# Kernel tuning notes

Measured on AMD Instinct MI355X. Metric: run time of the kernel, lower is better.

## Reference

```python
import jax, jax.numpy as jnp
import numpy as np

L, H, E, V, T_BLK = 8, 8, 768, 32000, 1024
B, T = 4, 1024
HS = E // H  # head size 96
STD = 0.02


def setup_inputs() -> dict:
    key = jax.random.key(0)
    ks = jax.random.split(key, 12)
    p = {}
    p["idx"] = jax.random.randint(ks[0], (B, T), 0, V)
    p["targets"] = jax.random.randint(ks[1], (B, T), 0, V)
    p["tok_emb"] = jax.random.normal(ks[2], (V, E), jnp.float32) * STD  # tied with lm_head
    p["pos_emb"] = jax.random.normal(ks[3], (T_BLK, E), jnp.float32) * STD
    p["Wq"] = jax.random.normal(ks[4], (L, E, E), jnp.float32) * STD
    p["Wk"] = jax.random.normal(ks[5], (L, E, E), jnp.float32) * STD
    p["Wv"] = jax.random.normal(ks[6], (L, E, E), jnp.float32) * STD
    p["Wo"] = jax.random.normal(ks[7], (L, E, E), jnp.float32) * STD
    p["bo"] = jnp.zeros((L, E), jnp.float32)
    p["ln1_g"] = jnp.ones((L, E), jnp.float32)
    p["ln1_b"] = jnp.zeros((L, E), jnp.float32)
    p["ln2_g"] = jnp.ones((L, E), jnp.float32)
    p["ln2_b"] = jnp.zeros((L, E), jnp.float32)
    p["W1"] = jax.random.normal(ks[8], (L, E, 4 * E), jnp.float32) * STD
    p["b1"] = jnp.zeros((L, 4 * E), jnp.float32)
    p["W2"] = jax.random.normal(ks[9], (L, 4 * E, E), jnp.float32) * STD
    p["b2"] = jnp.zeros((L, E), jnp.float32)
    p["lnf_g"] = jnp.ones((E,), jnp.float32)
    p["lnf_b"] = jnp.zeros((E,), jnp.float32)
    return p


def _ln(x, g, b):
    m = x.mean(-1, keepdims=True)
    v = ((x - m) ** 2).mean(-1, keepdims=True)
    return (x - m) * jax.lax.rsqrt(v + 1e-5) * g + b


def _attn(x, Wq, Wk, Wv, Wo, bo, mask):
    Bx, Tx, _ = x.shape
    q = (x @ Wq).reshape(Bx, Tx, H, HS)
    k = (x @ Wk).reshape(Bx, Tx, H, HS)
    v = (x @ Wv).reshape(Bx, Tx, H, HS)
    # per-head causal attention, scale by head_size**-0.5 as in source
    wei = jnp.einsum("bthd,bshd->bhts", q, k) * (HS ** -0.5)
    wei = jnp.where(mask, wei, -jnp.inf)
    wei = jax.nn.softmax(wei, axis=-1)
    out = jnp.einsum("bhts,bshd->bthd", wei, v).reshape(Bx, Tx, E)
    return out @ Wo + bo


def reference(idx, targets, tok_emb, pos_emb, Wq, Wk, Wv, Wo, bo,
              ln1_g, ln1_b, ln2_g, ln2_b, W1, b1, W2, b2, lnf_g, lnf_b):
    Tx = idx.shape[1]
    x = tok_emb[idx] + pos_emb[:Tx]  # [B,T,E]
    mask = jnp.tril(jnp.ones((Tx, Tx), bool))
    for l in range(L):
        x = x + _attn(_ln(x, ln1_g[l], ln1_b[l]), Wq[l], Wk[l], Wv[l], Wo[l], bo[l], mask)
        h = _ln(x, ln2_g[l], ln2_b[l])
        x = x + jax.nn.gelu(h @ W1[l] + b1[l], approximate=False) @ W2[l] + b2[l]
    x = _ln(x, lnf_g, lnf_b)
    logits = x @ tok_emb.T  # tied lm_head, [B,T,V]
    logp = jax.nn.log_softmax(logits, axis=-1)
    loss = -jnp.take_along_axis(logp, targets[..., None], axis=-1).mean()
    return logits, loss
```

## Files before the change

kernel.cpp:

```cpp
#include <hip/hip_runtime.h>
#include <cstdint>
#include <cstddef>


typedef __bf16 bf16_t;
typedef __bf16 bf16x8 __attribute__((ext_vector_type(8)));
typedef __bf16 bf16x4 __attribute__((ext_vector_type(4)));
typedef float  f32x4  __attribute__((ext_vector_type(4)));

#define LNUM 8
#define EMB 768
#define FFDIM 3072
#define HEADS 8
#define HSZ 96
#define VOC 32000
#define SEQ 1024
#define MTOK 4096
#define NT500 500

__device__ __forceinline__ void lds16(const void* g, void* l) {
    __builtin_amdgcn_global_load_lds(
        (__attribute__((address_space(1))) void*)(g),
        (__attribute__((address_space(3))) void*)(l), 16, 0, 0);
}

__global__ __launch_bounds__(256) void cast_bf16_kernel(
    const float* __restrict__ s, bf16_t* __restrict__ d, int n4)
{
    int i = blockIdx.x * 256 + threadIdx.x;
    if (i < n4) {
        float4 v = ((const float4*)s)[i];
        bf16x4 o;
        o[0] = (bf16_t)v.x; o[1] = (bf16_t)v.y;
        o[2] = (bf16_t)v.z; o[3] = (bf16_t)v.w;
        ((bf16x4*)d)[i] = o;
    }
}

__global__ __launch_bounds__(256) void transpose_cast_kernel(
    const float* __restrict__ src, bf16_t* __restrict__ dst,
    int K, int N, long long sstride, long long dstride)
{
    __shared__ float t[32][33];
    src += (long long)blockIdx.z * sstride;
    dst += (long long)blockIdx.z * dstride;
    int n0 = blockIdx.x * 32, k0 = blockIdx.y * 32;
    int tx = threadIdx.x, ty = threadIdx.y;
    for (int i = ty; i < 32; i += 8)
        t[i][tx] = src[(size_t)(k0 + i) * N + n0 + tx];
    __syncthreads();
    for (int i = ty; i < 32; i += 8)
        dst[(size_t)(n0 + i) * K + k0 + tx] = (bf16_t)t[tx][i];
}

__global__ __launch_bounds__(256) void embed_kernel(
    const int* __restrict__ idx, const float* __restrict__ tok,
    const float* __restrict__ pos, float* __restrict__ x)
{
    int row = blockIdx.x, tid = threadIdx.x;
    int id = idx[row];
    int t = row & (SEQ - 1);
    const float* te = tok + (size_t)id * EMB;
    const float* pe = pos + (size_t)t * EMB;
    float* xr = x + (size_t)row * EMB;
    xr[tid]       = te[tid]       + pe[tid];
    xr[tid + 256] = te[tid + 256] + pe[tid + 256];
    xr[tid + 512] = te[tid + 512] + pe[tid + 512];
}

__global__ __launch_bounds__(256) void ln_kernel(
    const float* __restrict__ x, const float* __restrict__ g,
    const float* __restrict__ bb, bf16_t* __restrict__ out)
{
    int row = blockIdx.x, tid = threadIdx.x;
    const float* xr = x + (size_t)row * EMB;
    float v0 = xr[tid], v1 = xr[tid + 256], v2 = xr[tid + 512];
    float s = v0 + v1 + v2;
    float s2 = v0 * v0 + v1 * v1 + v2 * v2;
#pragma unroll
    for (int off = 32; off >= 1; off >>= 1) {
        s  += __shfl_xor(s, off);
        s2 += __shfl_xor(s2, off);
    }
    __shared__ float red[8];
    int w = tid >> 6;
    if ((tid & 63) == 0) { red[w] = s; red[4 + w] = s2; }
    __syncthreads();
    s  = red[0] + red[1] + red[2] + red[3];
    s2 = red[4] + red[5] + red[6] + red[7];
    float mean = s * (1.0f / EMB);
    float var  = s2 * (1.0f / EMB) - mean * mean;
    float rs = rsqrtf(var + 1e-5f);
    bf16_t* orow = out + (size_t)row * EMB;
    orow[tid]       = (bf16_t)((v0 - mean) * rs * g[tid]       + bb[tid]);
    orow[tid + 256] = (bf16_t)((v1 - mean) * rs * g[tid + 256] + bb[tid + 256]);
    orow[tid + 512] = (bf16_t)((v2 - mean) * rs * g[tid + 512] + bb[tid + 512]);
}

__global__ __launch_bounds__(256) void gemm_nt_kernel(
    const bf16_t* __restrict__ A, const bf16_t* __restrict__ B,
    int N, int K, long long strideBz, long long strideOz,
    const float* __restrict__ bias, const float* __restrict__ resid,
    float* __restrict__ outF, bf16_t* __restrict__ outH, int gelu_flag,
    float* __restrict__ pmaxp, float* __restrict__ psump, int nt500)
{
    __shared__ __align__(16) bf16_t As[128 * 32];
    __shared__ __align__(16) bf16_t Bs[128 * 32];
    int tid = threadIdx.x;
    int m0 = blockIdx.y * 128;
    int n0 = blockIdx.x * 128;
    int z = blockIdx.z;
    B += (long long)z * strideBz;

    int wv = tid >> 6, lane = tid & 63;
    int quad = lane >> 4, l16 = lane & 15;
    int wm = wv >> 1, wn = wv & 1;

    const bf16_t* gA0 = A + (size_t)(m0 + (tid >> 2)) * K + (tid & 3) * 8;
    const bf16_t* gA1 = gA0 + (size_t)64 * K;
    const bf16_t* gB0 = B + (size_t)(n0 + (tid >> 2)) * K + (tid & 3) * 8;
    const bf16_t* gB1 = gB0 + (size_t)64 * K;
    bf16_t* lA0 = As + (wv << 9);
    bf16_t* lA1 = lA0 + 2048;
    bf16_t* lB0 = Bs + (wv << 9);
    bf16_t* lB1 = lB0 + 2048;

    f32x4 acc[4][4];
#pragma unroll
    for (int i = 0; i < 4; i++)
#pragma unroll
        for (int j = 0; j < 4; j++) {
            f32x4 zz = {0.f, 0.f, 0.f, 0.f};
            acc[i][j] = zz;
        }

    const bf16_t* fa = As + (wm * 64 + l16) * 32 + quad * 8;
    const bf16_t* fb = Bs + (wn * 64 + l16) * 32 + quad * 8;

    for (int kt = 0; kt < K; kt += 32) {
        lds16(gA0 + kt, lA0);
        lds16(gA1 + kt, lA1);
        lds16(gB0 + kt, lB0);
        lds16(gB1 + kt, lB1);
        __syncthreads();
        bf16x8 af[4], bfr[4];
#pragma unroll
        for (int i = 0; i < 4; i++) {
            af[i]  = *(const bf16x8*)(fa + i * 512);
            bfr[i] = *(const bf16x8*)(fb + i * 512);
        }
#pragma unroll
        for (int i = 0; i < 4; i++)
#pragma unroll
            for (int j = 0; j < 4; j++)
                acc[i][j] = __builtin_amdgcn_mfma_f32_16x16x32_bf16(
                    af[i], bfr[j], acc[i][j], 0, 0, 0);
        __syncthreads();
    }

    int mbase = m0 + wm * 64 + quad * 4;
    int nbase = n0 + wn * 64 + l16;

    if (outH) {
        bf16_t* oh = outH + (long long)z * strideOz;
#pragma unroll
        for (int i = 0; i < 4; i++)
#pragma unroll
            for (int j = 0; j < 4; j++) {
                int col = nbase + j * 16;
                float bv = bias ? bias[col] : 0.f;
#pragma unroll
                for (int r = 0; r < 4; r++) {
                    int row = mbase + i * 16 + r;
                    float v = acc[i][j][r] + bv;
                    if (gelu_flag)
                        v = 0.5f * v * (1.f + erff(v * 0.70710678118654752f));
                    oh[(size_t)row * N + col] = (bf16_t)v;
                }
            }
    } else {
#pragma unroll
        for (int i = 0; i < 4; i++)
#pragma unroll
            for (int j = 0; j < 4; j++) {
                int col = nbase + j * 16;
                float bv = bias ? bias[col] : 0.f;
#pragma unroll
                for (int r = 0; r < 4; r++) {
                    int row = mbase + i * 16 + r;
                    float v = acc[i][j][r] + bv;
                    if (resid) v += resid[(size_t)row * N + col];
                    outF[(size_t)row * N + col] = v;
                }
            }
        if (pmaxp) {
            int nt = blockIdx.x * 2 + wn;
#pragma unroll
            for (int i = 0; i < 4; i++)
#pragma unroll
                for (int r = 0; r < 4; r++) {
                    int row = mbase + i * 16 + r;
                    float mx = fmaxf(fmaxf(acc[i][0][r], acc[i][1][r]),
                                     fmaxf(acc[i][2][r], acc[i][3][r]));
                    mx = fmaxf(mx, __shfl_xor(mx, 1));
                    mx = fmaxf(mx, __shfl_xor(mx, 2));
                    mx = fmaxf(mx, __shfl_xor(mx, 4));
                    mx = fmaxf(mx, __shfl_xor(mx, 8));
                    float sm = 0.f;
#pragma unroll
                    for (int j = 0; j < 4; j++)
                        sm += __expf(acc[i][j][r] - mx);
                    sm += __shfl_xor(sm, 1);
                    sm += __shfl_xor(sm, 2);
                    sm += __shfl_xor(sm, 4);
                    sm += __shfl_xor(sm, 8);
                    if (l16 == 0) {
                        pmaxp[(size_t)row * nt500 + nt] = mx;
                        psump[(size_t)row * nt500 + nt] = sm;
                    }
                }
        }
    }
}

__global__ __launch_bounds__(256) void flash_kernel(
    const bf16_t* __restrict__ Qg, const bf16_t* __restrict__ Kg,
    const bf16_t* __restrict__ Vg, bf16_t* __restrict__ Og)
{
    __shared__ __align__(16) bf16_t Qs[64 * 96];
    __shared__ __align__(16) bf16_t Ks[64 * 96];
    __shared__ __align__(16) bf16_t Vt[96 * 72];
    __shared__ __align__(16) bf16_t Ps[64 * 72];

    int qt = blockIdx.x, bh = blockIdx.y;
    int b = bh >> 3, h = bh & 7;
    int tid = threadIdx.x;
    int wv = tid >> 6, lane = tid & 63;
    int quad = lane >> 4, l16 = lane & 15;
    size_t qrow0 = (size_t)b * SEQ + qt * 64;

    int cr[3], c8[3];
#pragma unroll
    for (int j = 0; j < 3; j++) {
        int c = wv * 192 + j * 64 + lane;
        cr[j] = c / 12;
        c8[j] = (c - cr[j] * 12) * 8;
    }

#pragma unroll
    for (int j = 0; j < 3; j++)
        lds16(Qg + (qrow0 + cr[j]) * EMB + h * HSZ + c8[j],
              Qs + (size_t)(wv * 192 + j * 64) * 8);

    const float scale = 0.10206207261596577f;

    f32x4 o[6];
#pragma unroll
    for (int dt = 0; dt < 6; dt++) { f32x4 z = {0.f, 0.f, 0.f, 0.f}; o[dt] = z; }
    float mrun[4], lrun[4];
#pragma unroll
    for (int r = 0; r < 4; r++) { mrun[r] = -1e30f; lrun[r] = 0.f; }

    bf16x8 qf[3];

    for (int kt = 0; kt <= qt; kt++) {
        size_t krow0 = (size_t)b * SEQ + kt * 64;
#pragma unroll
        for (int j = 0; j < 3; j++)
            lds16(Kg + (krow0 + cr[j]) * EMB + h * HSZ + c8[j],
                  Ks + (size_t)(wv * 192 + j * 64) * 8);
        bf16x8 vr[3];
#pragma unroll
        for (int j = 0; j < 3; j++)
            vr[j] = *(const bf16x8*)(Vg + (krow0 + cr[j]) * EMB + h * HSZ + c8[j]);
        __syncthreads();

        if (kt == 0) {
#pragma unroll
            for (int ks = 0; ks < 3; ks++)
                qf[ks] = *(const bf16x8*)(Qs + (wv * 16 + l16) * 96 + ks * 32 + quad * 8);
        }

#pragma unroll
        for (int j = 0; j < 3; j++)
#pragma unroll
            for (int e = 0; e < 8; e++)
                Vt[(c8[j] + e) * 72 + cr[j]] = vr[j][e];

        f32x4 s[4];
#pragma unroll
        for (int nt = 0; nt < 4; nt++) { f32x4 z = {0.f, 0.f, 0.f, 0.f}; s[nt] = z; }
#pragma unroll
        for (int ks = 0; ks < 3; ks++)
#pragma unroll
            for (int nt = 0; nt < 4; nt++) {
                bf16x8 kf = *(const bf16x8*)(Ks + (nt * 16 + l16) * 96 + ks * 32 + quad * 8);
                s[nt] = __builtin_amdgcn_mfma_f32_16x16x32_bf16(qf[ks], kf, s[nt], 0, 0, 0);
            }

        bool diag = (kt == qt);
        float p[4][4];
#pragma unroll
        for (int r = 0; r < 4; r++) {
            float sv[4];
#pragma unroll
            for (int nt = 0; nt < 4; nt++) {
                float v = s[nt][r] * scale;
                if (diag && (nt * 16 + l16 > wv * 16 + quad * 4 + r)) v = -1e30f;
                sv[nt] = v;
            }
            float mx = fmaxf(fmaxf(sv[0], sv[1]), fmaxf(sv[2], sv[3]));
            mx = fmaxf(mx, __shfl_xor(mx, 1));
            mx = fmaxf(mx, __shfl_xor(mx, 2));
            mx = fmaxf(mx, __shfl_xor(mx, 4));
            mx = fmaxf(mx, __shfl_xor(mx, 8));
            float mnew = fmaxf(mrun[r], mx);
            float al = __expf(mrun[r] - mnew);
            float sm = 0.f;
#pragma unroll
            for (int nt = 0; nt < 4; nt++) {
                float pv = __expf(sv[nt] - mnew);
                p[nt][r] = pv;
                sm += pv;
            }
            sm += __shfl_xor(sm, 1);
            sm += __shfl_xor(sm, 2);
            sm += __shfl_xor(sm, 4);
            sm += __shfl_xor(sm, 8);
            lrun[r] = lrun[r] * al + sm;
            mrun[r] = mnew;
#pragma unroll
            for (int dt = 0; dt < 6; dt++) o[dt][r] *= al;
        }

#pragma unroll
        for (int nt = 0; nt < 4; nt++)
#pragma unroll
            for (int r = 0; r < 4; r++)
                Ps[(wv * 16 + quad * 4 + r) * 72 + nt * 16 + l16] = (bf16_t)p[nt][r];

        __syncthreads();

#pragma unroll
        for (int ks = 0; ks < 2; ks++) {
            bf16x8 pf = *(const bf16x8*)(Ps + (wv * 16 + l16) * 72 + ks * 32 + quad * 8);
#pragma unroll
            for (int dt = 0; dt < 6; dt++) {
                bf16x8 vf = *(const bf16x8*)(Vt + (dt * 16 + l16) * 72 + ks * 32 + quad * 8);
                o[dt] = __builtin_amdgcn_mfma_f32_16x16x32_bf16(pf, vf, o[dt], 0, 0, 0);
            }
        }
    }

#pragma unroll
    for (int r = 0; r < 4; r++) {
        float inv = 1.f / lrun[r];
        size_t row = qrow0 + wv * 16 + quad * 4 + r;
#pragma unroll
        for (int dt = 0; dt < 6; dt++)
            Og[row * EMB + h * HSZ + dt * 16 + l16] = (bf16_t)(o[dt][r] * inv);
    }
}

__global__ __launch_bounds__(256) void loss_rows_kernel(
    const float* __restrict__ pmax, const float* __restrict__ psum,
    const float* __restrict__ logits, const int* __restrict__ tgt,
    float* __restrict__ rl)
{
    int row = blockIdx.x, tid = threadIdx.x;
    const float* pm = pmax + (size_t)row * NT500;
    const float* ps = psum + (size_t)row * NT500;
    float mx = -1e30f;
    for (int i = tid; i < NT500; i += 256) mx = fmaxf(mx, pm[i]);
#pragma unroll
    for (int off = 32; off >= 1; off >>= 1) mx = fmaxf(mx, __shfl_xor(mx, off));
    __shared__ float red[8];
    int w = tid >> 6;
    if ((tid & 63) == 0) red[w] = mx;
    __syncthreads();
    mx = fmaxf(fmaxf(red[0], red[1]), fmaxf(red[2], red[3]));
    float sm = 0.f;
    for (int i = tid; i < NT500; i += 256) sm += ps[i] * __expf(pm[i] - mx);
#pragma unroll
    for (int off = 32; off >= 1; off >>= 1) sm += __shfl_xor(sm, off);
    if ((tid & 63) == 0) red[4 + w] = sm;
    __syncthreads();
    if (tid == 0) {
        float tot = red[4] + red[5] + red[6] + red[7];
        float lse = mx + logf(tot);
        float tl = logits[(size_t)row * VOC + tgt[row]];
        rl[row] = lse - tl;
    }
}

__global__ __launch_bounds__(256) void loss_final_kernel(
    const float* __restrict__ rl, float* __restrict__ dst)
{
    int tid = threadIdx.x;
    float s = 0.f;
    for (int i = tid; i < MTOK; i += 256) s += rl[i];
#pragma unroll
    for (int off = 32; off >= 1; off >>= 1) s += __shfl_xor(s, off);
    __shared__ float red[4];
    if ((tid & 63) == 0) red[tid >> 6] = s;
    __syncthreads();
    if (tid == 0)
        dst[0] = (red[0] + red[1] + red[2] + red[3]) * (1.0f / MTOK);
}

extern "C" void kernel_launch(void* const* d_in, const int* in_sizes, int n_in,
                              void* d_out, int out_size, void* d_ws, size_t ws_size,
                              hipStream_t stream)
{
    (void)in_sizes; (void)n_in;
    const int*   idx  = (const int*)d_in[0];
    const int*   tgt  = (const int*)d_in[1];
    const float* tok  = (const float*)d_in[2];
    const float* pos  = (const float*)d_in[3];
    const float* Wq   = (const float*)d_in[4];
    const float* Wk   = (const float*)d_in[5];
    const float* Wv   = (const float*)d_in[6];
    const float* Wo   = (const float*)d_in[7];
    const float* bo   = (const float*)d_in[8];
    const float* ln1g = (const float*)d_in[9];
    const float* ln1b = (const float*)d_in[10];
    const float* ln2g = (const float*)d_in[11];
    const float* ln2b = (const float*)d_in[12];
    const float* W1   = (const float*)d_in[13];
    const float* b1   = (const float*)d_in[14];
    const float* W2   = (const float*)d_in[15];
    const float* b2   = (const float*)d_in[16];
    const float* lnfg = (const float*)d_in[17];
    const float* lnfb = (const float*)d_in[18];
    float* logits = (float*)d_out;

    char* ws = (char*)d_ws;
    constexpr size_t EE  = (size_t)EMB * EMB;
    constexpr size_t ACT = (size_t)MTOK * EMB;
    constexpr size_t EF  = (size_t)EMB * FFDIM;

    float*  Xf    = (float*) (ws + 0);
    bf16_t* LnO   = (bf16_t*)(ws + 12582912);
    bf16_t* QKV   = (bf16_t*)(ws + 18874368);
    bf16_t* AtO   = (bf16_t*)(ws + 37748736);
    bf16_t* Ffh   = (bf16_t*)(ws + 44040192);
    bf16_t* WqkvT = (bf16_t*)(ws + 69206016);
    bf16_t* WoT   = (bf16_t*)(ws + 97517568);
    bf16_t* W1T   = (bf16_t*)(ws + 106954752);
    bf16_t* W2T   = (bf16_t*)(ws + 144703488);
    bf16_t* EmbB  = (bf16_t*)(ws + 182452224);
    float*  Pmax  = (float*) (ws + 231604224);
    float*  Psum  = (float*) (ws + 239796224);
    float*  Rloss = (float*) (ws + 247988224);
    if (ws_size < (size_t)248004608) return;

    dim3 tb(32, 8);
    cast_bf16_kernel<<<24000, 256, 0, stream>>>(tok, EmbB, (VOC * EMB) / 4);
    transpose_cast_kernel<<<dim3(24, 24, 8), tb, 0, stream>>>(
        Wq, WqkvT + 0 * EE, EMB, EMB, (long long)EE, (long long)(3 * EE));
    transpose_cast_kernel<<<dim3(24, 24, 8), tb, 0, stream>>>(
        Wk, WqkvT + 1 * EE, EMB, EMB, (long long)EE, (long long)(3 * EE));
    transpose_cast_kernel<<<dim3(24, 24, 8), tb, 0, stream>>>(
        Wv, WqkvT + 2 * EE, EMB, EMB, (long long)EE, (long long)(3 * EE));
    transpose_cast_kernel<<<dim3(24, 24, 8), tb, 0, stream>>>(
        Wo, WoT, EMB, EMB, (long long)EE, (long long)EE);
    transpose_cast_kernel<<<dim3(96, 24, 8), tb, 0, stream>>>(
        W1, W1T, EMB, FFDIM, (long long)EF, (long long)EF);
    transpose_cast_kernel<<<dim3(24, 96, 8), tb, 0, stream>>>(
        W2, W2T, FFDIM, EMB, (long long)EF, (long long)EF);

    embed_kernel<<<MTOK, 256, 0, stream>>>(idx, tok, pos, Xf);

    for (int l = 0; l < LNUM; l++) {
        ln_kernel<<<MTOK, 256, 0, stream>>>(Xf, ln1g + l * EMB, ln1b + l * EMB, LnO);
        gemm_nt_kernel<<<dim3(6, 32, 3), 256, 0, stream>>>(
            LnO, WqkvT + (size_t)l * 3 * EE, EMB, EMB,
            (long long)EE, (long long)ACT,
            nullptr, nullptr, nullptr, QKV, 0, nullptr, nullptr, 0);
        flash_kernel<<<dim3(16, 32), 256, 0, stream>>>(
            QKV, QKV + ACT, QKV + 2 * ACT, AtO);
        gemm_nt_kernel<<<dim3(6, 32, 1), 256, 0, stream>>>(
            AtO, WoT + (size_t)l * EE, EMB, EMB, 0, 0,
            bo + l * EMB, Xf, Xf, nullptr, 0, nullptr, nullptr, 0);
        ln_kernel<<<MTOK, 256, 0, stream>>>(Xf, ln2g + l * EMB, ln2b + l * EMB, LnO);
        gemm_nt_kernel<<<dim3(24, 32, 1), 256, 0, stream>>>(
            LnO, W1T + (size_t)l * EF, FFDIM, EMB, 0, 0,
            b1 + l * FFDIM, nullptr, nullptr, Ffh, 1, nullptr, nullptr, 0);
        gemm_nt_kernel<<<dim3(6, 32, 1), 256, 0, stream>>>(
            Ffh, W2T + (size_t)l * EF, EMB, FFDIM, 0, 0,
            b2 + l * EMB, Xf, Xf, nullptr, 0, nullptr, nullptr, 0);
    }

    ln_kernel<<<MTOK, 256, 0, stream>>>(Xf, lnfg, lnfb, LnO);
    gemm_nt_kernel<<<dim3(250, 32, 1), 256, 0, stream>>>(
        LnO, EmbB, VOC, EMB, 0, 0,
        nullptr, nullptr, logits, nullptr, 0, Pmax, Psum, NT500);
    loss_rows_kernel<<<MTOK, 256, 0, stream>>>(Pmax, Psum, logits, tgt, Rloss);
    loss_final_kernel<<<1, 256, 0, stream>>>(Rloss, logits + ((size_t)out_size - 1));
}
```

Before: 3.716 ms.

## Double-buffer GEMM LDS tiles and reorder LM-head grid for weight reuse

The GEMM main loop now uses two LDS buffers. The next K-tile is loaded asynchronously while the current one is computed, with explicit vmcnt waits and barriers replacing the old load-sync-compute-sync pattern. The LM-head GEMM also switches to an M-first grid so consecutive blocks share the same embedding-weight tile, which should improve L2 reuse. LDS use doubles, which may lower occupancy.

New measurement: 3.214 ms. 13.5% less time.

```diff
diff --git a/kernel.cpp b/kernel.cpp
--- a/kernel.cpp
+++ b/kernel.cpp
@@ -102,13 +102,14 @@
     int N, int K, long long strideBz, long long strideOz,
     const float* __restrict__ bias, const float* __restrict__ resid,
     float* __restrict__ outF, bf16_t* __restrict__ outH, int gelu_flag,
-    float* __restrict__ pmaxp, float* __restrict__ psump, int nt500)
-{
-    __shared__ __align__(16) bf16_t As[128 * 32];
-    __shared__ __align__(16) bf16_t Bs[128 * 32];
+    float* __restrict__ pmaxp, float* __restrict__ psump, int nt500, int mfirst)
+{
+    __shared__ __align__(16) bf16_t As[2 * 128 * 32];
+    __shared__ __align__(16) bf16_t Bs[2 * 128 * 32];
     int tid = threadIdx.x;
-    int m0 = blockIdx.y * 128;
-    int n0 = blockIdx.x * 128;
+    int m0, n0, ntcol;
+    if (mfirst) { m0 = blockIdx.x * 128; n0 = blockIdx.y * 128; ntcol = blockIdx.y; }
+    else        { n0 = blockIdx.x * 128; m0 = blockIdx.y * 128; ntcol = blockIdx.x; }
     int z = blockIdx.z;
     B += (long long)z * strideBz;
 
@@ -120,10 +121,6 @@
     const bf16_t* gA1 = gA0 + (size_t)64 * K;
     const bf16_t* gB0 = B + (size_t)(n0 + (tid >> 2)) * K + (tid & 3) * 8;
     const bf16_t* gB1 = gB0 + (size_t)64 * K;
-    bf16_t* lA0 = As + (wv << 9);
-    bf16_t* lA1 = lA0 + 2048;
-    bf16_t* lB0 = Bs + (wv << 9);
-    bf16_t* lB1 = lB0 + 2048;
 
     f32x4 acc[4][4];
 #pragma unroll
@@ -137,17 +134,22 @@
     const bf16_t* fa = As + (wm * 64 + l16) * 32 + quad * 8;
     const bf16_t* fb = Bs + (wn * 64 + l16) * 32 + quad * 8;
 
-    for (int kt = 0; kt < K; kt += 32) {
-        lds16(gA0 + kt, lA0);
-        lds16(gA1 + kt, lA1);
-        lds16(gB0 + kt, lB0);
-        lds16(gB1 + kt, lB1);
-        __syncthreads();
+    auto stage = [&](int bb, int kt) {
+        bf16_t* dA = As + (bb << 12) + (wv << 9);
+        bf16_t* dB = Bs + (bb << 12) + (wv << 9);
+        lds16(gA0 + kt, dA);
+        lds16(gA1 + kt, dA + 2048);
+        lds16(gB0 + kt, dB);
+        lds16(gB1 + kt, dB + 2048);
+    };
+    auto compute = [&](int bb) {
+        const bf16_t* fa_c = fa + (bb << 12);
+        const bf16_t* fb_c = fb + (bb << 12);
         bf16x8 af[4], bfr[4];
 #pragma unroll
         for (int i = 0; i < 4; i++) {
-            af[i]  = *(const bf16x8*)(fa + i * 512);
-            bfr[i] = *(const bf16x8*)(fb + i * 512);
+            af[i]  = *(const bf16x8*)(fa_c + i * 512);
+            bfr[i] = *(const bf16x8*)(fb_c + i * 512);
         }
 #pragma unroll
         for (int i = 0; i < 4; i++)
@@ -155,7 +157,27 @@
             for (int j = 0; j < 4; j++)
                 acc[i][j] = __builtin_amdgcn_mfma_f32_16x16x32_bf16(
                     af[i], bfr[j], acc[i][j], 0, 0, 0);
-        __syncthreads();
+    };
+
+    int nsteps = K >> 5;
+    stage(0, 0);
+    if (nsteps > 1) stage(1, 32);
+    for (int t = 0; t < nsteps - 1; ++t) {
+        int cur = t & 1;
+        asm volatile("s_waitcnt vmcnt(4)" ::: "memory");
+        __builtin_amdgcn_s_barrier();
+        __builtin_amdgcn_sched_barrier(0);
+        compute(cur);
+        __builtin_amdgcn_sched_barrier(0);
+        __builtin_amdgcn_s_barrier();
+        if (t + 2 < nsteps) stage(cur, (t + 2) << 5);
+    }
+    {
+        int cur = (nsteps - 1) & 1;
+        asm volatile("s_waitcnt vmcnt(0)" ::: "memory");
+        __builtin_amdgcn_s_barrier();
+        __builtin_amdgcn_sched_barrier(0);
+        compute(cur);
     }
 
     int mbase = m0 + wm * 64 + quad * 4;
@@ -194,7 +216,7 @@
                 }
             }
         if (pmaxp) {
-            int nt = blockIdx.x * 2 + wn;
+            int nt = ntcol * 2 + wn;
 #pragma unroll
             for (int i = 0; i < 4; i++)
 #pragma unroll
@@ -476,25 +498,25 @@
         gemm_nt_kernel<<<dim3(6, 32, 3), 256, 0, stream>>>(
             LnO, WqkvT + (size_t)l * 3 * EE, EMB, EMB,
             (long long)EE, (long long)ACT,
-            nullptr, nullptr, nullptr, QKV, 0, nullptr, nullptr, 0);
+            nullptr, nullptr, nullptr, QKV, 0, nullptr, nullptr, 0, 0);
         flash_kernel<<<dim3(16, 32), 256, 0, stream>>>(
             QKV, QKV + ACT, QKV + 2 * ACT, AtO);
         gemm_nt_kernel<<<dim3(6, 32, 1), 256, 0, stream>>>(
             AtO, WoT + (size_t)l * EE, EMB, EMB, 0, 0,
-            bo + l * EMB, Xf, Xf, nullptr, 0, nullptr, nullptr, 0);
+            bo + l * EMB, Xf, Xf, nullptr, 0, nullptr, nullptr, 0, 0);
         ln_kernel<<<MTOK, 256, 0, stream>>>(Xf, ln2g + l * EMB, ln2b + l * EMB, LnO);
         gemm_nt_kernel<<<dim3(24, 32, 1), 256, 0, stream>>>(
             LnO, W1T + (size_t)l * EF, FFDIM, EMB, 0, 0,
-            b1 + l * FFDIM, nullptr, nullptr, Ffh, 1, nullptr, nullptr, 0);
+            b1 + l * FFDIM, nullptr, nullptr, Ffh, 1, nullptr, nullptr, 0, 0);
         gemm_nt_kernel<<<dim3(6, 32, 1), 256, 0, stream>>>(
             Ffh, W2T + (size_t)l * EF, EMB, FFDIM, 0, 0,
-            b2 + l * EMB, Xf, Xf, nullptr, 0, nullptr, nullptr, 0);
+            b2 + l * EMB, Xf, Xf, nullptr, 0, nullptr, nullptr, 0, 0);
     }
 
     ln_kernel<<<MTOK, 256, 0, stream>>>(Xf, lnfg, lnfb, LnO);
-    gemm_nt_kernel<<<dim3(250, 32, 1), 256, 0, stream>>>(
+    gemm_nt_kernel<<<dim3(32, 250, 1), 256, 0, stream>>>(
         LnO, EmbB, VOC, EMB, 0, 0,
-        nullptr, nullptr, logits, nullptr, 0, Pmax, Psum, NT500);
+        nullptr, nullptr, logits, nullptr, 0, Pmax, Psum, NT500, 1);
     loss_rows_kernel<<<MTOK, 256, 0, stream>>>(Pmax, Psum, logits, tgt, Rloss);
     loss_final_kernel<<<1, 256, 0, stream>>>(Rloss, logits + ((size_t)out_size - 1));
 }
```
